# Kernel tuning notes

Hardware: AMD Instinct MI355X
Metric: run time of the kernel (lower is better)

The kernel has to match this reference:

```python
import jax, jax.numpy as jnp
import numpy as np

EPS = 1e-8

def _l2norm(x):
    # normalize rows, guarding against zero norm like torch cosine similarity eps
    n = jnp.sqrt(jnp.sum(x * x, axis=-1, keepdims=True))
    return x / jnp.maximum(n, EPS)

def setup_inputs() -> dict:
    key = jax.random.key(0)
    k1, k2, k3 = jax.random.split(key, 3)
    Nq, Nk, D = 4096, 4096, 1024
    return {
        "queries": jax.random.normal(k1, (Nq, D), dtype=jnp.float32),
        "keys": jax.random.normal(k2, (Nk, D), dtype=jnp.float32),
        "values": jax.random.normal(k3, (Nk, D), dtype=jnp.float32),
    }

def reference(queries, keys, values):
    # CosineSimilarityMatrix(keys, queries): [Nk, Nq] pairwise cosine sims
    attn_weights = jnp.matmul(_l2norm(keys), _l2norm(queries).T)  # [Nk, Nq]
    # weighted sum over keys for each query
    weighted = jnp.matmul(attn_weights.T, values)  # [Nq, D]
    return (weighted, attn_weights)
```

## Files before the change

kernel.cpp:

```cpp
#include <hip/hip_runtime.h>


typedef unsigned short u16;
typedef unsigned int u32;
typedef unsigned char u8;
typedef float f32x4 __attribute__((ext_vector_type(4)));
typedef int int4v __attribute__((ext_vector_type(4)));
typedef __bf16 bf16x8 __attribute__((ext_vector_type(8)));

__device__ __forceinline__ u16 f2bf(float f) {
  u32 u = __builtin_bit_cast(u32, f);
  return (u16)((u + 0x7FFFu + ((u >> 16) & 1u)) >> 16);
}

__device__ __forceinline__ void gload16(const u16* g, u16* l) {
  __builtin_amdgcn_global_load_lds((__attribute__((address_space(1))) void*)(void*)g,
                                   (__attribute__((address_space(3))) void*)(void*)l, 16, 0, 0);
}
__device__ __forceinline__ void gload16b(const u8* g, u8* l) {
  __builtin_amdgcn_global_load_lds((__attribute__((address_space(1))) void*)(void*)g,
                                   (__attribute__((address_space(3))) void*)(void*)l, 16, 0, 0);
}

#define BARRIER() __builtin_amdgcn_s_barrier()
#define WAITVM(n) asm volatile("s_waitcnt vmcnt(" #n ")" ::: "memory")
#define WAITLGKM0() do { asm volatile("s_waitcnt lgkmcnt(0)" ::: "memory"); \
                         __builtin_amdgcn_sched_barrier(0); } while (0)

__global__ __launch_bounds__(256) void norm_transv_kernel(
    const float* __restrict__ q, const float* __restrict__ k,
    u16* __restrict__ qnb, u16* __restrict__ knb,
    u8* __restrict__ qnq, u8* __restrict__ knq,
    float* __restrict__ sclQ, float* __restrict__ sclK,
    const float* __restrict__ v, u16* __restrict__ vbT) {
  int bid = blockIdx.x, t = threadIdx.x;
  if (bid < 8192) {
    const bool isQ = (bid < 4096);
    const float* src = isQ ? q : k;
    u16* dst = isQ ? qnb : knb;
    u8* dst8 = isQ ? qnq : knq;
    float* scl = isQ ? sclQ : sclK;
    int row = bid & 4095;
    const float4 val = ((const float4*)(src + (size_t)row * 1024))[t];
    float s = val.x * val.x + val.y * val.y + val.z * val.z + val.w * val.w;
    float am = fmaxf(fmaxf(fabsf(val.x), fabsf(val.y)), fmaxf(fabsf(val.z), fabsf(val.w)));
    #pragma unroll
    for (int off = 32; off > 0; off >>= 1) {
      s += __shfl_xor(s, off, 64);
      am = fmaxf(am, __shfl_xor(am, off, 64));
    }
    __shared__ float2 red[4];
    if ((t & 63) == 0) red[t >> 6] = make_float2(s, am);
    __syncthreads();
    float tot = red[0].x + red[1].x + red[2].x + red[3].x;
    float amall = fmaxf(fmaxf(red[0].y, red[1].y), fmaxf(red[2].y, red[3].y));
    float inv = 1.0f / fmaxf(sqrtf(tot), 1e-8f);
    float rm = fmaxf(amall * inv, 1e-30f);
    float iq = 127.0f / rm;
    uint2 o;
    o.x = (u32)f2bf(val.x * inv) | ((u32)f2bf(val.y * inv) << 16);
    o.y = (u32)f2bf(val.z * inv) | ((u32)f2bf(val.w * inv) << 16);
    *(uint2*)(dst + (size_t)row * 1024 + t * 4) = o;
    int c0 = (int)rintf(val.x * inv * iq);
    int c1 = (int)rintf(val.y * inv * iq);
    int c2 = (int)rintf(val.z * inv * iq);
    int c3 = (int)rintf(val.w * inv * iq);
    u32 p = (u32)(c0 & 255) | ((u32)(c1 & 255) << 8) |
            ((u32)(c2 & 255) << 16) | ((u32)(c3 & 255) << 24);
    ((u32*)(dst8 + (size_t)row * 1024))[t] = p;
    if (t == 0) scl[row] = rm * (1.0f / 127.0f);
  } else {
    __shared__ __align__(16) float lds[64 * 64];
    int tix = bid - 8192;
    int r0 = (tix >> 4) * 64, c0 = (tix & 15) * 64;
    int ch = t & 15, lr = t >> 4;
    #pragma unroll
    for (int i = 0; i < 4; ++i) {
      int r = lr + i * 16;
      float4 val = *(const float4*)&v[(size_t)(r0 + r) * 1024 + c0 + ch * 4];
      int byteoff = r * 256 + ((ch * 16) ^ (((r >> 3) & 7) << 4));
      *(float4*)((char*)lds + byteoff) = val;
    }
    __syncthreads();
    int cch = t & 7, lrow = t >> 3;
    #pragma unroll
    for (int i = 0; i < 2; ++i) {
      int oc = lrow + i * 32;
      u16 vals[8];
      #pragma unroll
      for (int j = 0; j < 8; ++j) {
        int srl = cch * 8 + j;
        int byteoff = srl * 256 + (((oc >> 2) * 16) ^ (((srl >> 3) & 7) << 4)) + (oc & 3) * 4;
        vals[j] = f2bf(*(const float*)((const char*)lds + byteoff));
      }
      uint4 o;
      o.x = (u32)vals[0] | ((u32)vals[1] << 16);
      o.y = (u32)vals[2] | ((u32)vals[3] << 16);
      o.z = (u32)vals[4] | ((u32)vals[5] << 16);
      o.w = (u32)vals[6] | ((u32)vals[7] << 16);
      *(uint4*)&vbT[(size_t)(c0 + oc) * 4096 + r0 + cch * 8] = o;
    }
  }
}

__global__ __launch_bounds__(256) void transpose_bf16_kernel(
    const u16* __restrict__ src, u16* __restrict__ dst) {
  int b = blockIdx.x;
  int r0 = (b >> 4) * 64, c0 = (b & 15) * 64;
  __shared__ __align__(16) u16 lds[64 * 64];
  int t = threadIdx.x;
  int lrow = t >> 3, cch = t & 7;
  #pragma unroll
  for (int i = 0; i < 2; ++i) {
    int sr = lrow + i * 32;
    uint4 val = *(const uint4*)&src[(size_t)(r0 + sr) * 1024 + c0 + cch * 8];
    int byteoff = sr * 128 + ((cch * 16) ^ (((sr >> 3) & 7) << 4));
    *(uint4*)((char*)lds + byteoff) = val;
  }
  __syncthreads();
  #pragma unroll
  for (int i = 0; i < 2; ++i) {
    int oc = lrow + i * 32;
    u16 vals[8];
    #pragma unroll
    for (int j = 0; j < 8; ++j) {
      int srl = cch * 8 + j;
      int byteoff = srl * 128 + ((oc * 2) ^ (cch << 4));
      vals[j] = *(const u16*)((const char*)lds + byteoff);
    }
    uint4 o;
    o.x = (u32)vals[0] | ((u32)vals[1] << 16);
    o.y = (u32)vals[2] | ((u32)vals[3] << 16);
    o.z = (u32)vals[4] | ((u32)vals[5] << 16);
    o.w = (u32)vals[6] | ((u32)vals[7] << 16);
    *(uint4*)&dst[(size_t)(c0 + oc) * 4096 + r0 + cch * 8] = o;
  }
}

template<int BM, int BN, int MW, int NW>
__global__ __launch_bounds__(256) void gemm_abt(
    const u16* __restrict__ A, const u16* __restrict__ B, float* __restrict__ Cptr,
    int k_len, int lda, int ldb, int ldc, int plane) {
  static_assert(BM == 2 * MW * 16 && BN == 2 * NW * 16, "wave grid is 2x2");
  static_assert(BM / 32 + BN / 32 == 6, "WAITVM(6) literal assumes 6 loads/thread/stage");
  constexpr int TILE = (BM + BN) * 64;
  __shared__ __align__(16) u16 lds[3 * TILE];
  const int t = threadIdx.x, l = t & 63, w = t >> 6;
  const int tileM = blockIdx.y, tileN = blockIdx.x;
  const int k_start = blockIdx.z * k_len;
  Cptr += (size_t)blockIdx.z * plane;
  const int srow = l >> 3;
  const int cswz = ((l & 7) ^ srow) * 8;
  const u16* gA = A + (size_t)(tileM * BM) * lda + k_start + cswz;
  const u16* gB = B + (size_t)(tileN * BN) * ldb + k_start + cswz;
  const int slot0 = (l >> 4) ^ (l & 7);
  const int aoff0 = ((w >> 1) * MW * 16 + (l & 15)) * 64 + slot0 * 8;
  const int aoff1 = ((w >> 1) * MW * 16 + (l & 15)) * 64 + (slot0 ^ 4) * 8;
  const int boff0 = BM * 64 + ((w & 1) * NW * 16 + (l & 15)) * 64 + slot0 * 8;
  const int boff1 = BM * 64 + ((w & 1) * NW * 16 + (l & 15)) * 64 + (slot0 ^ 4) * 8;

  f32x4 acc[MW][NW];
  #pragma unroll
  for (int m = 0; m < MW; ++m)
    #pragma unroll
    for (int n = 0; n < NW; ++n) acc[m][n] = (f32x4){0.f, 0.f, 0.f, 0.f};

  auto stage = [&](int buf, int kof) {
    u16* bb = lds + buf * TILE;
    #pragma unroll
    for (int j = 0; j < BM / 32; ++j) {
      const int r = w * (BM / 4) + j * 8;
      gload16(gA + (size_t)(r + srow) * lda + kof, bb + r * 64);
    }
    #pragma unroll
    for (int j = 0; j < BN / 32; ++j) {
      const int r = w * (BN / 4) + j * 8;
      gload16(gB + (size_t)(r + srow) * ldb + kof, bb + BM * 64 + r * 64);
    }
  };

  bf16x8 av0[MW], bv0[NW], av1[MW], bv1[NW];
  const int nt = k_len >> 6;
  stage(0, 0);
  if (nt > 1) { stage(1, 64); WAITVM(6); }
  else        { WAITVM(0); }
  BARRIER();
  #pragma unroll
  for (int m = 0; m < MW; ++m) av0[m] = *(const bf16x8*)&lds[aoff0 + m * 1024];
  #pragma unroll
  for (int n = 0; n < NW; ++n) bv0[n] = *(const bf16x8*)&lds[boff0 + n * 1024];

  for (int i = 0; i < nt; ++i) {
    const u16* bb = lds + (i % 3) * TILE;
    if (i + 2 < nt) stage((i + 2) % 3, (i + 2) * 64);
    #pragma unroll
    for (int m = 0; m < MW; ++m) av1[m] = *(const bf16x8*)&bb[aoff1 + m * 1024];
    #pragma unroll
    for (int n = 0; n < NW; ++n) bv1[n] = *(const bf16x8*)&bb[boff1 + n * 1024];
    #pragma unroll
    for (int m = 0; m < MW; ++m)
      #pragma unroll
      for (int n = 0; n < NW; ++n)
        acc[m][n] = __builtin_amdgcn_mfma_f32_16x16x32_bf16(av0[m], bv0[n], acc[m][n], 0, 0, 0);
    #pragma unroll
    for (int m = 0; m < MW; ++m)
      #pragma unroll
      for (int n = 0; n < NW; ++n)
        acc[m][n] = __builtin_amdgcn_mfma_f32_16x16x32_bf16(av1[m], bv1[n], acc[m][n], 0, 0, 0);
    if (i + 1 < nt) {
      if (i + 2 < nt) { WAITVM(6); } else { WAITVM(0); }
    }
    BARRIER();
    if (i + 1 < nt) {
      const u16* nb = lds + ((i + 1) % 3) * TILE;
      #pragma unroll
      for (int m = 0; m < MW; ++m) av0[m] = *(const bf16x8*)&nb[aoff0 + m * 1024];
      #pragma unroll
      for (int n = 0; n < NW; ++n) bv0[n] = *(const bf16x8*)&nb[boff0 + n * 1024];
    }
  }

  const int orow = tileM * BM + (w >> 1) * MW * 16 + (l >> 4) * 4;
  const int ocol = tileN * BN + (w & 1) * NW * 16 + (l & 15);
  #pragma unroll
  for (int m = 0; m < MW; ++m)
    #pragma unroll
    for (int n = 0; n < NW; ++n)
      #pragma unroll
      for (int r = 0; r < 4; ++r)
        Cptr[(size_t)(orow + m * 16 + r) * ldc + (ocol + n * 16)] = acc[m][n][r];
}

__global__ __launch_bounds__(512, 2) void gemm256_i8(
    const u8* __restrict__ A8, const u8* __restrict__ B8, float* __restrict__ C,
    const float* __restrict__ P, u16* __restrict__ ctred,
    const float* __restrict__ sclK, const float* __restrict__ sclQ, int ntn) {
  __shared__ __align__(16) u8 lds8[131072];
  const int tid = threadIdx.x, l = tid & 63, w = tid >> 6;
  const int wm = w >> 2, wn = w & 3;
  const int nwg = gridDim.x * gridDim.y;
  const int bid = blockIdx.y * gridDim.x + blockIdx.x;
  const int swz = (bid & 7) * (nwg >> 3) + (bid >> 3);
  const int tileM = swz / ntn, tileN = swz % ntn;

  const int r0 = w * 32 + (l >> 2);
  const int s0 = ((l & 3) ^ ((l >> 3) & 3)) * 16;
  const int offA = r0 * 1024 + s0;
  const u8* gA8 = A8 + (size_t)tileM * 256 * 1024;
  const u8* gB8 = B8 + (size_t)tileN * 256 * 1024;

#define STGA8(kof, bb) do { \
    gload16b(gA8 + (kof) + offA,          lds8 + (bb) + w * 2048); \
    gload16b(gA8 + (kof) + offA + 16384,  lds8 + (bb) + w * 2048 + 1024); } while (0)
#define STGB8(kof, bb) do { \
    gload16b(gB8 + (kof) + offA,          lds8 + (bb) + 16384 + w * 2048); \
    gload16b(gB8 + (kof) + offA + 16384,  lds8 + (bb) + 16384 + w * 2048 + 1024); } while (0)

  STGA8(0, 0);        STGB8(0, 0);
  STGA8(64, 32768);   STGB8(64, 32768);
  STGA8(128, 65536);  STGB8(128, 65536);
  STGA8(192, 98304);  STGB8(192, 98304);
  {
    const int base = bid * 4096 + tid * 8;
    f32x4 sa = *(const f32x4*)&P[base];
    f32x4 sb = *(const f32x4*)&P[base + 4];
    #pragma unroll
    for (int p = 1; p < 4; ++p) {
      sa += *(const f32x4*)&P[(size_t)p * 1048576 + base];
      sb += *(const f32x4*)&P[(size_t)p * 1048576 + base + 4];
    }
    uint4 o;
    o.x = (u32)f2bf(sa[0]) | ((u32)f2bf(sa[1]) << 16);
    o.y = (u32)f2bf(sa[2]) | ((u32)f2bf(sa[3]) << 16);
    o.z = (u32)f2bf(sb[0]) | ((u32)f2bf(sb[1]) << 16);
    o.w = (u32)f2bf(sb[2]) | ((u32)f2bf(sb[3]) << 16);
    *(uint4*)&ctred[base] = o;
  }
  WAITVM(0);
  BARRIER();

  const int scol = ((l >> 4) ^ ((l >> 1) & 3)) * 16;
  const int afragB = (wm * 128 + (l & 15)) * 64 + scol;
  const int bfragB = (wn * 64 + (l & 15)) * 64 + scol;

  int4v acc[8][4];
  #pragma unroll
  for (int m = 0; m < 8; ++m)
    #pragma unroll
    for (int n = 0; n < 4; ++n) acc[m][n] = (int4v){0, 0, 0, 0};

  int4v A0[4], A1[4], B0[4];
  #pragma unroll
  for (int m = 0; m < 4; ++m) A0[m] = *(const int4v*)&lds8[afragB + m * 1024];
  #pragma unroll
  for (int n = 0; n < 4; ++n) B0[n] = *(const int4v*)&lds8[16384 + bfragB + n * 1024];

  const int NT = 16;
  for (int t = 0; t < NT; ++t) {
    const int bb = (t & 3) * 32768;
    const int koff = t * 64;
    #pragma unroll
    for (int m = 0; m < 4; ++m) A1[m] = *(const int4v*)&lds8[bb + afragB + (m + 4) * 1024];
    BARRIER();
    WAITLGKM0();
    __builtin_amdgcn_s_setprio(1);
    #pragma unroll
    for (int m = 0; m < 4; ++m)
      #pragma unroll
      for (int n = 0; n < 4; ++n)
        acc[m][n] = __builtin_amdgcn_mfma_i32_16x16x64_i8(A0[m], B0[n], acc[m][n], 0, 0, 0);
    __builtin_amdgcn_s_setprio(0);
    BARRIER();
    if (t + 4 < NT) { STGA8(koff + 256, bb); STGB8(koff + 256, bb); }
    __builtin_amdgcn_s_setprio(1);
    #pragma unroll
    for (int m = 0; m < 4; ++m)
      #pragma unroll
      for (int n = 0; n < 4; ++n)
        acc[m + 4][n] = __builtin_amdgcn_mfma_i32_16x16x64_i8(A1[m], B0[n], acc[m + 4][n], 0, 0, 0);
    __builtin_amdgcn_s_setprio(0);
    if (t + 4 < NT)      { WAITVM(12); }
    else if (t + 3 < NT) { WAITVM(8); }
    else if (t + 2 < NT) { WAITVM(4); }
    else if (t + 1 < NT) { WAITVM(0); }
    BARRIER();
    if (t + 1 < NT) {
      const int nb = ((t + 1) & 3) * 32768;
      #pragma unroll
      for (int m = 0; m < 4; ++m) A0[m] = *(const int4v*)&lds8[nb + afragB + m * 1024];
      #pragma unroll
      for (int n = 0; n < 4; ++n) B0[n] = *(const int4v*)&lds8[nb + 16384 + bfragB + n * 1024];
    }
  }

  const int orow = tileM * 256 + wm * 128 + (l >> 4) * 4;
  const int ocol = tileN * 256 + wn * 64 + (l & 15);
  float sq[4];
  #pragma unroll
  for (int n = 0; n < 4; ++n) sq[n] = sclQ[ocol + n * 16];
  #pragma unroll
  for (int m = 0; m < 8; ++m) {
    const float4 sk4 = *(const float4*)&sclK[orow + m * 16];
    #pragma unroll
    for (int n = 0; n < 4; ++n)
      #pragma unroll
      for (int r = 0; r < 4; ++r)
        C[(size_t)(orow + m * 16 + r) * 4096 + (ocol + n * 16)] =
            (float)acc[m][n][r] * ((const float*)&sk4)[r] * sq[n];
  }
#undef STGA8
#undef STGB8
}

extern "C" void kernel_launch(void* const* d_in, const int* in_sizes, int n_in,
                              void* d_out, int out_size, void* d_ws, size_t ws_size,
                              hipStream_t stream) {
  const float* q = (const float*)d_in[0];
  const float* k = (const float*)d_in[1];
  const float* v = (const float*)d_in[2];
  float* out = (float*)d_out;
  float* weighted = out;
  float* attn = out + 4194304;

  char* ws = (char*)d_ws;
  u16* qnb = (u16*)(ws);
  u16* knb = (u16*)(ws + (8u << 20));
  u16* knT = (u16*)(ws + (16u << 20));
  u16* vbT = (u16*)(ws + (24u << 20));
  u16* ct  = (u16*)(ws + (32u << 20));
  u8*  qnq = (u8*)(ws + (34u << 20));
  u8*  knq = (u8*)(ws + (38u << 20));
  float* sclQ = (float*)(ws + (42u << 20));
  float* sclK = (float*)(ws + (42u << 20) + 65536);

  norm_transv_kernel<<<9216, 256, 0, stream>>>(q, k, qnb, knb, qnq, knq, sclQ, sclK, v, vbT);
  transpose_bf16_kernel<<<1024, 256, 0, stream>>>(knb, knT);
  gemm_abt<128, 64, 4, 2><<<dim3(16, 8, 4), 256, 0, stream>>>(
      vbT, knT, weighted, 1024, 4096, 4096, 1024, 1048576);
  gemm256_i8<<<dim3(16, 16), 512, 0, stream>>>(
      knq, qnq, attn, weighted, ct, sclK, sclQ, 16);
  gemm_abt<128, 64, 4, 2><<<dim3(16, 32, 1), 256, 0, stream>>>(
      qnb, ct, weighted, 1024, 1024, 1024, 1024, 0);
}
```

Before: 83.58 us.

## Restructure int8 GEMM mainloop to double-buffered 128-wide K tiles

The int8 attention-weight GEMM mainloop changes from a four-stage ring of 64-byte K slices to a two-stage double buffer of 128-byte K slices, cutting the iteration count from 16 to 8. Global-to-LDS loads for the next tile are split into four chunks interleaved between the MFMA groups. The LDS layout and XOR swizzle change to fit 128-byte rows. Each iteration now has one barrier instead of three, but the prefetch depth drops to one tile and there is a full vmcnt(0) wait before every barrier, which could expose memory latency.

```diff
diff --git a/kernel.cpp b/kernel.cpp
--- a/kernel.cpp
+++ b/kernel.cpp
@@ -243,23 +243,18 @@
   const int swz = (bid & 7) * (nwg >> 3) + (bid >> 3);
   const int tileM = swz / ntn, tileN = swz % ntn;
 
-  const int r0 = w * 32 + (l >> 2);
-  const int s0 = ((l & 3) ^ ((l >> 3) & 3)) * 16;
-  const int offA = r0 * 1024 + s0;
-  const u8* gA8 = A8 + (size_t)tileM * 256 * 1024;
-  const u8* gB8 = B8 + (size_t)tileN * 256 * 1024;
-
-#define STGA8(kof, bb) do { \
-    gload16b(gA8 + (kof) + offA,          lds8 + (bb) + w * 2048); \
-    gload16b(gA8 + (kof) + offA + 16384,  lds8 + (bb) + w * 2048 + 1024); } while (0)
-#define STGB8(kof, bb) do { \
-    gload16b(gB8 + (kof) + offA,          lds8 + (bb) + 16384 + w * 2048); \
-    gload16b(gB8 + (kof) + offA + 16384,  lds8 + (bb) + 16384 + w * 2048 + 1024); } while (0)
-
-  STGA8(0, 0);        STGB8(0, 0);
-  STGA8(64, 32768);   STGB8(64, 32768);
-  STGA8(128, 65536);  STGB8(128, 65536);
-  STGA8(192, 98304);  STGB8(192, 98304);
+  const int srow8 = l >> 3;
+  const int cswzB = ((l & 7) ^ srow8) * 16;
+  const u8* gA8 = A8 + (size_t)tileM * 256 * 1024 + cswzB;
+  const u8* gB8 = B8 + (size_t)tileN * 256 * 1024 + cswzB;
+
+#define STGJ(j, koff, bb) do { \
+    gload16b(gA8 + (size_t)(w * 8 + 64 * (j) + srow8) * 1024 + (koff), \
+             lds8 + (bb) + w * 1024 + (j) * 8192); \
+    gload16b(gB8 + (size_t)(w * 8 + 64 * (j) + srow8) * 1024 + (koff), \
+             lds8 + (bb) + 32768 + w * 1024 + (j) * 8192); } while (0)
+
+  STGJ(0, 0, 0); STGJ(1, 0, 0); STGJ(2, 0, 0); STGJ(3, 0, 0);
   {
     const int base = bid * 4096 + tid * 8;
     f32x4 sa = *(const f32x4*)&P[base];
@@ -279,9 +274,9 @@
   WAITVM(0);
   BARRIER();
 
-  const int scol = ((l >> 4) ^ ((l >> 1) & 3)) * 16;
-  const int afragB = (wm * 128 + (l & 15)) * 64 + scol;
-  const int bfragB = (wn * 64 + (l & 15)) * 64 + scol;
+  const int fs = ((l >> 4) ^ (l & 7)) * 16;
+  const int afrag0 = (wm * 128 + (l & 15)) * 128 + fs;
+  const int bfrag0 = 32768 + (wn * 64 + (l & 15)) * 128 + fs;
 
   int4v acc[8][4];
   #pragma unroll
@@ -289,47 +284,52 @@
     #pragma unroll
     for (int n = 0; n < 4; ++n) acc[m][n] = (int4v){0, 0, 0, 0};
 
-  int4v A0[4], A1[4], B0[4];
-  #pragma unroll
-  for (int m = 0; m < 4; ++m) A0[m] = *(const int4v*)&lds8[afragB + m * 1024];
-  #pragma unroll
-  for (int n = 0; n < 4; ++n) B0[n] = *(const int4v*)&lds8[16384 + bfragB + n * 1024];
-
-  const int NT = 16;
+#define MFMA16(AF, BF, MB) do { \
+    __builtin_amdgcn_s_setprio(1); \
+    _Pragma("unroll") \
+    for (int m = 0; m < 4; ++m) { \
+      _Pragma("unroll") \
+      for (int n = 0; n < 4; ++n) \
+        acc[(MB) + m][n] = __builtin_amdgcn_mfma_i32_16x16x64_i8(AF[m], BF[n], acc[(MB) + m][n], 0, 0, 0); \
+    } \
+    __builtin_amdgcn_s_setprio(0); } while (0)
+
+  int4v A0[4], A1[4], B0[4], B1[4];
+  #pragma unroll
+  for (int m = 0; m < 4; ++m) A0[m] = *(const int4v*)&lds8[afrag0 + m * 2048];
+  #pragma unroll
+  for (int n = 0; n < 4; ++n) B0[n] = *(const int4v*)&lds8[bfrag0 + n * 2048];
+
+  const int NT = 8;
   for (int t = 0; t < NT; ++t) {
-    const int bb = (t & 3) * 32768;
-    const int koff = t * 64;
-    #pragma unroll
-    for (int m = 0; m < 4; ++m) A1[m] = *(const int4v*)&lds8[bb + afragB + (m + 4) * 1024];
-    BARRIER();
+    const int bb = (t & 1) << 16, nb = bb ^ 65536;
+    const int nkoff = (t + 1) * 128;
+    if (t + 1 < NT) STGJ(0, nkoff, nb);
+    #pragma unroll
+    for (int m = 0; m < 4; ++m) A1[m] = *(const int4v*)&lds8[bb + (afrag0 + (m + 4) * 2048)];
     WAITLGKM0();
-    __builtin_amdgcn_s_setprio(1);
-    #pragma unroll
-    for (int m = 0; m < 4; ++m)
-      #pragma unroll
-      for (int n = 0; n < 4; ++n)
-        acc[m][n] = __builtin_amdgcn_mfma_i32_16x16x64_i8(A0[m], B0[n], acc[m][n], 0, 0, 0);
-    __builtin_amdgcn_s_setprio(0);
-    BARRIER();
-    if (t + 4 < NT) { STGA8(koff + 256, bb); STGB8(koff + 256, bb); }
-    __builtin_amdgcn_s_setprio(1);
-    #pragma unroll
-    for (int m = 0; m < 4; ++m)
-      #pragma unroll
-      for (int n = 0; n < 4; ++n)
-        acc[m + 4][n] = __builtin_amdgcn_mfma_i32_16x16x64_i8(A1[m], B0[n], acc[m + 4][n], 0, 0, 0);
-    __builtin_amdgcn_s_setprio(0);
-    if (t + 4 < NT)      { WAITVM(12); }
-    else if (t + 3 < NT) { WAITVM(8); }
-    else if (t + 2 < NT) { WAITVM(4); }
-    else if (t + 1 < NT) { WAITVM(0); }
-    BARRIER();
+    MFMA16(A0, B0, 0);
+    if (t + 1 < NT) STGJ(1, nkoff, nb);
+    #pragma unroll
+    for (int m = 0; m < 4; ++m) A0[m] = *(const int4v*)&lds8[bb + ((afrag0 ^ 64) + m * 2048)];
+    #pragma unroll
+    for (int n = 0; n < 4; ++n) B1[n] = *(const int4v*)&lds8[bb + ((bfrag0 ^ 64) + n * 2048)];
+    WAITLGKM0();
+    MFMA16(A1, B0, 4);
+    if (t + 1 < NT) STGJ(2, nkoff, nb);
+    #pragma unroll
+    for (int m = 0; m < 4; ++m) A1[m] = *(const int4v*)&lds8[bb + ((afrag0 ^ 64) + (m + 4) * 2048)];
+    WAITLGKM0();
+    MFMA16(A0, B1, 0);
+    if (t + 1 < NT) STGJ(3, nkoff, nb);
+    MFMA16(A1, B1, 4);
     if (t + 1 < NT) {
-      const int nb = ((t + 1) & 3) * 32768;
-      #pragma unroll
-      for (int m = 0; m < 4; ++m) A0[m] = *(const int4v*)&lds8[nb + afragB + m * 1024];
-      #pragma unroll
-      for (int n = 0; n < 4; ++n) B0[n] = *(const int4v*)&lds8[nb + 16384 + bfragB + n * 1024];
+      WAITVM(0);
+      BARRIER();
+      #pragma unroll
+      for (int m = 0; m < 4; ++m) A0[m] = *(const int4v*)&lds8[nb + (afrag0 + m * 2048)];
+      #pragma unroll
+      for (int n = 0; n < 4; ++n) B0[n] = *(const int4v*)&lds8[nb + (bfrag0 + n * 2048)];
     }
   }
 
@@ -348,8 +348,8 @@
         C[(size_t)(orow + m * 16 + r) * 4096 + (ocol + n * 16)] =
             (float)acc[m][n][r] * ((const float*)&sk4)[r] * sq[n];
   }
-#undef STGA8
-#undef STGB8
+#undef STGJ
+#undef MFMA16
 }
 
 extern "C" void kernel_launch(void* const* d_in, const int* in_sizes, int n_in,
```

Measured after the change: 82.50 us. Within noise of the previous version (-1.3%).
